# Optimization experiments

Measured on AMD Instinct MI355X. Metric: run time of the kernel, lower is better.

Reference implementation:

```python
import jax, jax.numpy as jnp
import numpy as np

B, IMG, C = 128, 128, 3
NP = 8                      # n_patches per side
PS = IMG // NP              # patch size = 16
IN_D = C * PS * PS          # 768
E, NH, L, A = 768, 12, 12, 256
HS = E // NH                # 64
T = NP * NP + 1             # 65 tokens (cls + patches)
LN_EPS = 1e-5


def _pos_emb(seq_len, d):
    i = np.arange(seq_len, dtype=np.float64)[:, None]
    j = np.arange(d, dtype=np.float64)[None, :]
    even = np.sin(i / 10000 ** (j / d))
    odd = np.cos(i / 10000 ** ((j - 1) / d))
    return jnp.asarray(np.where(j % 2 == 0, even, odd), dtype=jnp.float32)


def setup_inputs() -> dict:
    key = jax.random.key(0)
    ks = jax.random.split(key, 16)
    s_e = 1.0 / np.sqrt(E)
    s_in = 1.0 / np.sqrt(IN_D)
    s_4e = 1.0 / np.sqrt(4 * E)
    return {
        "images": jax.random.normal(ks[0], (B, IMG, IMG, C), jnp.float32),
        "lin_w": jax.random.normal(ks[1], (IN_D, E), jnp.float32) * s_in,
        "cls_tok": jax.random.uniform(ks[2], (1, E), jnp.float32),
        "pos_emb": _pos_emb(T, E),
        "Wq": jax.random.normal(ks[3], (L, E, E), jnp.float32) * s_e,
        "Wk": jax.random.normal(ks[4], (L, E, E), jnp.float32) * s_e,
        "Wv": jax.random.normal(ks[5], (L, E, E), jnp.float32) * s_e,
        "Wo": jax.random.normal(ks[6], (L, E, E), jnp.float32) * s_e,
        "bo": jnp.zeros((L, E), jnp.float32),
        "ln1g": jnp.ones((L, E), jnp.float32),
        "ln1b": jnp.zeros((L, E), jnp.float32),
        "ln2g": jnp.ones((L, E), jnp.float32),
        "ln2b": jnp.zeros((L, E), jnp.float32),
        "W1": jax.random.normal(ks[7], (L, E, 4 * E), jnp.float32) * s_e,
        "b1": jnp.zeros((L, 4 * E), jnp.float32),
        "W2": jax.random.normal(ks[8], (L, 4 * E, E), jnp.float32) * s_4e,
        "b2": jnp.zeros((L, E), jnp.float32),
        "head_w": jax.random.normal(ks[9], (E, A), jnp.float32) * s_e,
        "head_b": jnp.zeros((A,), jnp.float32),
    }


def _layernorm(x, g, b):
    mu = jnp.mean(x, axis=-1, keepdims=True)
    var = jnp.var(x, axis=-1, keepdims=True)
    return (x - mu) * jax.lax.rsqrt(var + LN_EPS) * g + b


def _vit_forward(images, lin_w, cls_tok, pos_emb, Wq, Wk, Wv, Wo, bo,
                 ln1g, ln1b, ln2g, ln2b, W1, b1, W2, b2, head_w, head_b):
    n = images.shape[0]
    # patches: 'b (h p1) (w p2) c -> b (h w) (p1 p2 c)'
    p = images.reshape(n, NP, PS, NP, PS, C)
    patches = p.transpose(0, 1, 3, 2, 4, 5).reshape(n, NP * NP, IN_D)
    x = patches @ lin_w                                   # [B, 64, E]
    x = jnp.concatenate([jnp.broadcast_to(cls_tok, (n, 1, E)), x], axis=1)
    x = x + pos_emb[None]                                 # [B, T, E]

    scale = E ** (-0.5)  # NOTE: original scales by n_embd, not head_size

    def block(x, params):
        wq, wk, wv, wo_, bo_, g1, be1, g2, be2, w1, bb1, w2, bb2 = params
        h = _layernorm(x, g1, be1)
        q = (h @ wq).reshape(n, T, NH, HS)
        k = (h @ wk).reshape(n, T, NH, HS)
        v = (h @ wv).reshape(n, T, NH, HS)
        wei = jnp.einsum('bthd,bshd->bhts', q, k) * scale
        wei = jax.nn.softmax(wei, axis=-1)
        attn = jnp.einsum('bhts,bshd->bthd', wei, v).reshape(n, T, E)
        x = x + attn @ wo_ + bo_
        h2 = _layernorm(x, g2, be2)
        x = x + jax.nn.relu(h2 @ w1 + bb1) @ w2 + bb2
        return x, None

    x, _ = jax.lax.scan(block, x,
                        (Wq, Wk, Wv, Wo, bo, ln1g, ln1b, ln2g, ln2b,
                         W1, b1, W2, b2))
    cls = x[:, 0]                                          # [B, E]
    logits = jax.nn.softmax(cls @ head_w + head_b, axis=-1)  # model ends in Softmax
    return logits


def reference(images, lin_w, cls_tok, pos_emb, Wq, Wk, Wv, Wo, bo,
              ln1g, ln1b, ln2g, ln2b, W1, b1, W2, b2, head_w, head_b):
    return _vit_forward(images, lin_w, cls_tok, pos_emb, Wq, Wk, Wv, Wo, bo,
                        ln1g, ln1b, ln2g, ln2b, W1, b1, W2, b2, head_w, head_b)
```

## Files before the change

### kernel.cpp

```cpp
#include <hip/hip_runtime.h>
#include <cstdint>
#include <cstddef>


typedef __bf16 bf16x8 __attribute__((ext_vector_type(8)));
typedef float  f32x4  __attribute__((ext_vector_type(4)));

#define DEVINL __device__ __forceinline__

DEVINL uint16_t f2bf(float f){
  union U{float f; uint32_t i;} v; v.f=f; uint32_t u=v.i;
  return (uint16_t)((u + 0x7fffu + ((u>>16)&1u)) >> 16);
}

DEVINL void gl_lds16(const void* g, void* l){
  __builtin_amdgcn_global_load_lds((const __attribute__((address_space(1))) void*)g,
                                   (__attribute__((address_space(3))) void*)l, 16, 0, 0);
}

__global__ __launch_bounds__(256) void patchify_k(const float* __restrict__ img,
                                                  uint16_t* __restrict__ out){
  int i = blockIdx.x*256 + threadIdx.x;
  int m  = i / 768, kk = i - m*768;
  int b  = m >> 6,  t  = m & 63;
  int py = t >> 3,  px = t & 7;
  int r  = kk / 48, rem = kk - r*48;
  size_t src = ((size_t)(b*128 + py*16 + r)*128 + px*16)*3 + rem;
  out[i] = f2bf(img[src]);
}

DEVINL void tile_transpose(const float* __restrict__ src, uint16_t* __restrict__ dst,
                           int R, int C, int ti, int tj, int tid){
  __shared__ uint16_t tile[32][33];
  int tx = tid & 31, ty = tid >> 5;
  int r0 = ti*32, c0 = tj*32;
  #pragma unroll
  for (int i=0;i<4;++i)
    tile[ty+i*8][tx] = f2bf(src[(size_t)(r0+ty+i*8)*C + c0 + tx]);
  __syncthreads();
  #pragma unroll
  for (int i=0;i<4;++i)
    dst[(size_t)(c0+ty+i*8)*R + r0 + tx] = tile[tx][ty+i*8];
}

__global__ __launch_bounds__(256) void transpose_cvt_k(const float* __restrict__ src,
                                                       uint16_t* __restrict__ dst, int R, int C){
  tile_transpose(src, dst, R, C, blockIdx.y, blockIdx.x, threadIdx.x);
}

__global__ __launch_bounds__(256) void prep_layer_k(
    const float* __restrict__ Wq, const float* __restrict__ Wk,
    const float* __restrict__ Wv, const float* __restrict__ Wo,
    const float* __restrict__ W1, const float* __restrict__ W2,
    uint16_t* __restrict__ wbuf){
  int idx = blockIdx.x;
  const float* src; uint16_t* dst; int R, C, ti, tj;
  if (idx < 2304){
    int m = idx / 576, t = idx - m*576; ti = t/24; tj = t - ti*24; R=768; C=768;
    src = (m==0)?Wq:(m==1)?Wk:(m==2)?Wv:Wo;
    dst = wbuf + (size_t)m*589824;
  } else if (idx < 4608){
    int t = idx - 2304; ti = t/96; tj = t - ti*96; R=768; C=3072;
    src = W1; dst = wbuf + 2359296;
  } else {
    int t = idx - 4608; ti = t/24; tj = t - ti*24; R=3072; C=768;
    src = W2; dst = wbuf + 4718592;
  }
  tile_transpose(src, dst, R, C, ti, tj, threadIdx.x);
}

__global__ __launch_bounds__(256) void cls_init_k(const float* __restrict__ ct,
                                                  const float* __restrict__ pos,
                                                  float* __restrict__ X){
  int b = blockIdx.x, tid = threadIdx.x;
  for (int e = tid; e < 768; e += 256)
    X[(size_t)b*65*768 + e] = ct[e] + pos[e];
}

__global__ __launch_bounds__(256) void ln_k(const float* __restrict__ Xin,
                                            uint16_t* __restrict__ H,
                                            const float* __restrict__ g,
                                            const float* __restrict__ b){
  int row = blockIdx.x, tid = threadIdx.x;
  const float* xr = Xin + (size_t)row*768;
  float v0 = xr[tid], v1 = xr[tid+256], v2 = xr[tid+512];
  int wid = tid>>6, lane = tid&63;
  __shared__ float part[4];
  __shared__ float bc[2];
  float s = v0+v1+v2;
  #pragma unroll
  for (int o=32;o;o>>=1) s += __shfl_down(s,o);
  if (lane==0) part[wid] = s;
  __syncthreads();
  if (tid==0) bc[0] = (part[0]+part[1]+part[2]+part[3]) * (1.f/768.f);
  __syncthreads();
  float mu = bc[0];
  float d0=v0-mu, d1=v1-mu, d2=v2-mu;
  float q = d0*d0 + d1*d1 + d2*d2;
  #pragma unroll
  for (int o=32;o;o>>=1) q += __shfl_down(q,o);
  __syncthreads();
  if (lane==0) part[wid] = q;
  __syncthreads();
  if (tid==0) bc[1] = rsqrtf((part[0]+part[1]+part[2]+part[3])*(1.f/768.f) + 1e-5f);
  __syncthreads();
  float rs = bc[1];
  uint16_t* hr = H + (size_t)row*768;
  hr[tid]     = f2bf(d0*rs*g[tid]     + b[tid]);
  hr[tid+256] = f2bf(d1*rs*g[tid+256] + b[tid+256]);
  hr[tid+512] = f2bf(d2*rs*g[tid+512] + b[tid+512]);
}

enum { EP_BF16=0, EP_RES=1, EP_RELU=2, EP_EMB=3 };

template<int MODE, int BN>
__global__ __launch_bounds__(256) void gemm_bt_k(
    const uint16_t* __restrict__ A, const uint16_t* __restrict__ Bt,
    int M, int N, int K, int strideB, long long strideO,
    const float* __restrict__ bias, float* __restrict__ X,
    uint16_t* __restrict__ Obf, const float* __restrict__ pos)
{
  constexpr int WN = BN/2;
  constexpr int NF = WN/16;
  constexpr int BLOADS = BN/64;
  __shared__ __align__(16) uint16_t sA[2][128*32];
  __shared__ __align__(16) uint16_t sB[2][BN*32];
  const int tid = threadIdx.x;
  const int wid = tid>>6, lane = tid&63;
  const int nx = gridDim.x;
  const int nwg = nx*gridDim.y;
  {
  }
  int idx = blockIdx.y*nx + blockIdx.x;
  int q8 = nwg>>3, r8 = nwg&7, xcd = idx&7, off = idx>>3;
  int swz = (xcd<r8 ? xcd*(q8+1) : r8*(q8+1) + (xcd-r8)*q8) + off;
  const int bn = (swz % nx)*BN, bm = (swz / nx)*128;
  const int z = blockIdx.z;
  const uint16_t* Bz = Bt + (size_t)z*strideB;
  const int wr = wid>>1, wc = wid&1;
  const int frow = lane&15, g = lane>>4;
  int srA[2], scA[2];
  #pragma unroll
  for (int rr=0; rr<2; ++rr){
    int G = rr*256 + tid;
    srA[rr] = G>>2; scA[rr] = ((G&3) - (G>>3)) & 3;
  }
  int srB[2], scB[2];
  #pragma unroll
  for (int rr=0; rr<BLOADS; ++rr){
    int G = rr*256 + tid;
    srB[rr] = G>>2; scB[rr] = ((G&3) - (G>>3)) & 3;
  }
  const int rsw = (frow>>1)&3;
  f32x4 acc[4][NF] = {};
  const int nt = K>>5;

  #pragma unroll
  for (int rr=0; rr<2; ++rr)
    gl_lds16(A + (size_t)(bm+srA[rr])*K + scA[rr]*8, (char*)sA[0] + (rr*256 + wid*64)*16);
  #pragma unroll
  for (int rr=0; rr<BLOADS; ++rr)
    gl_lds16(Bz + (size_t)(bn+srB[rr])*K + scB[rr]*8, (char*)sB[0] + (rr*256 + wid*64)*16);

  int buf = 0;
  for (int t = 0; t < nt; ++t){
    if (t+1 < nt){
      int k0 = (t+1)<<5;
      #pragma unroll
      for (int rr=0; rr<2; ++rr)
        gl_lds16(A + (size_t)(bm+srA[rr])*K + k0 + scA[rr]*8,
                 (char*)sA[buf^1] + (rr*256 + wid*64)*16);
      #pragma unroll
      for (int rr=0; rr<BLOADS; ++rr)
        gl_lds16(Bz + (size_t)(bn+srB[rr])*K + k0 + scB[rr]*8,
                 (char*)sB[buf^1] + (rr*256 + wid*64)*16);
      if constexpr (BLOADS==1) asm volatile("s_waitcnt vmcnt(3)" ::: "memory");
      else                     asm volatile("s_waitcnt vmcnt(4)" ::: "memory");
    } else {
      asm volatile("s_waitcnt vmcnt(0)" ::: "memory");
    }
    __builtin_amdgcn_s_barrier();
    bf16x8 a[4], b[NF];
    const char* sAc = (const char*)sA[buf];
    const char* sBc = (const char*)sB[buf];
    #pragma unroll
    for (int m=0;m<4;++m)
      a[m] = *(const bf16x8*)(sAc + (wr*64+m*16+frow)*64 + (((g+rsw)&3)<<4));
    #pragma unroll
    for (int n=0;n<NF;++n)
      b[n] = *(const bf16x8*)(sBc + (wc*WN+n*16+frow)*64 + (((g+rsw)&3)<<4));
    #pragma unroll
    for (int m=0;m<4;++m)
      #pragma unroll
      for (int n=0;n<NF;++n)
        acc[m][n] = __builtin_amdgcn_mfma_f32_16x16x32_bf16(a[m], b[n], acc[m][n], 0,0,0);
    __builtin_amdgcn_s_barrier();
    buf ^= 1;
  }

  uint16_t* Oz = Obf + (size_t)z*(size_t)strideO;
  #pragma unroll
  for (int m=0;m<4;++m){
    int gr0 = bm + wr*64 + m*16 + (lane>>4)*4;
    #pragma unroll
    for (int n=0;n<NF;++n){
      int gc = bn + wc*WN + n*16 + (lane&15);
      #pragma unroll
      for (int r=0;r<4;++r){
        int grow = gr0 + r;
        float vsum = acc[m][n][r];
        if constexpr (MODE==EP_BF16){
          Oz[(size_t)grow*N + gc] = f2bf(vsum);
        } else if constexpr (MODE==EP_RES){
          X[(size_t)grow*N + gc] += vsum + bias[gc];
        } else if constexpr (MODE==EP_RELU){
          float u = vsum + bias[gc];
          Oz[(size_t)grow*N + gc] = f2bf(u > 0.f ? u : 0.f);
        } else {
          int t2 = grow & 63, bb = grow >> 6;
          X[((size_t)bb*65 + 1 + t2)*768 + gc] = vsum + pos[(size_t)(t2+1)*768 + gc];
        }
      }
    }
  }
}

__global__ __launch_bounds__(320) void attn_mfma_k(const uint16_t* __restrict__ q,
    const uint16_t* __restrict__ k, const uint16_t* __restrict__ v,
    uint16_t* __restrict__ o)
{
  __shared__ __align__(16) uint16_t P_lds[80][104];
  __shared__ __align__(16) uint16_t Vt[64][104];
  const int bh = blockIdx.x; const int b = bh / 12, hd = bh - b*12;
  const int tid = threadIdx.x;
  const int m = tid>>6;
  const int lane = tid&63;
  const int g = lane>>4, c = lane&15;
  const size_t base = (size_t)b*65*768 + (size_t)hd*64;

  for (int i = tid; i < 80*16; i += 320) P_lds[i>>4][80 + (i&15)] = 0;
  for (int i = tid; i < 64*32; i += 320) Vt[i>>5][64 + (i&31)] = 0;
  __syncthreads();
  for (int j = tid; j < 520; j += 320){
    int key = j >> 3, dc = j & 7;
    union { bf16x8 v8; uint16_t u[8]; } gv;
    gv.v8 = *(const bf16x8*)&v[base + (size_t)key*768 + dc*8];
    #pragma unroll
    for (int e = 0; e < 8; ++e) Vt[dc*8 + e][key] = gv.u[e];
  }

  bf16x8 bk[5][2];
  #pragma unroll
  for (int n=0;n<5;++n)
    #pragma unroll
    for (int kk=0;kk<2;++kk)
      bk[n][kk] = *(const bf16x8*)&k[base + (size_t)(n*16 + c)*768 + kk*32 + g*8];

  bf16x8 aq[2];
  #pragma unroll
  for (int kk=0;kk<2;++kk)
    aq[kk] = *(const bf16x8*)&q[base + (size_t)(m*16 + c)*768 + kk*32 + g*8];
  f32x4 sacc[5] = {};
  #pragma unroll
  for (int kk=0;kk<2;++kk)
    #pragma unroll
    for (int n=0;n<5;++n)
      sacc[n] = __builtin_amdgcn_mfma_f32_16x16x32_bf16(aq[kk], bk[n][kk], sacc[n], 0,0,0);

  const float scale = 0.03608439182435161f;
  #pragma unroll
  for (int r=0;r<4;++r){
    float val[5]; float mx = -3.0e38f;
    #pragma unroll
    for (int n=0;n<5;++n){
      val[n] = (n*16 + c) < 65 ? sacc[n][r]*scale : -3.0e38f;
      mx = fmaxf(mx, val[n]);
    }
    #pragma unroll
    for (int off=1; off<16; off<<=1) mx = fmaxf(mx, __shfl_xor(mx, off));
    float p[5], sum = 0.f;
    #pragma unroll
    for (int n=0;n<5;++n){
      p[n] = (n*16 + c) < 65 ? __expf(val[n]-mx) : 0.f;
      sum += p[n];
    }
    #pragma unroll
    for (int off=1; off<16; off<<=1) sum += __shfl_xor(sum, off);
    float rinv = 1.f / sum;
    int row = m*16 + g*4 + r;
    #pragma unroll
    for (int n=0;n<5;++n) P_lds[row][n*16 + c] = f2bf(p[n]*rinv);
  }
  __syncthreads();

  bf16x8 vb[4][3];
  #pragma unroll
  for (int n=0;n<4;++n)
    #pragma unroll
    for (int kk=0;kk<3;++kk)
      vb[n][kk] = *(const bf16x8*)&Vt[n*16 + c][kk*32 + g*8];
  f32x4 oacc[4] = {};
  #pragma unroll
  for (int kk=0;kk<3;++kk){
    bf16x8 pa = *(const bf16x8*)&P_lds[m*16 + c][kk*32 + g*8];
    #pragma unroll
    for (int n=0;n<4;++n)
      oacc[n] = __builtin_amdgcn_mfma_f32_16x16x32_bf16(pa, vb[n][kk], oacc[n], 0,0,0);
  }
  #pragma unroll
  for (int r=0;r<4;++r){
    int row = m*16 + g*4 + r;
    if (row < 65){
      #pragma unroll
      for (int n=0;n<4;++n)
        o[base + (size_t)row*768 + n*16 + c] = f2bf(oacc[n][r]);
    }
  }
}

__global__ __launch_bounds__(256) void head_k(const float* __restrict__ X,
    const float* __restrict__ W, const float* __restrict__ bias,
    float* __restrict__ out){
  int b = blockIdx.x, a = threadIdx.x;
  const float* xr = X + (size_t)b*65*768;
  float acc = bias[a];
  for (int kk=0; kk<768; ++kk) acc += xr[kk]*W[(size_t)kk*256 + a];
  int wid = a>>6, lane = a&63;
  __shared__ float red[4];
  float mx = acc;
  #pragma unroll
  for (int off=32; off; off>>=1) mx = fmaxf(mx, __shfl_xor(mx, off));
  if (lane==0) red[wid]=mx;
  __syncthreads();
  mx = fmaxf(fmaxf(red[0],red[1]), fmaxf(red[2],red[3]));
  float e = __expf(acc-mx);
  float s = e;
  #pragma unroll
  for (int off=32; off; off>>=1) s += __shfl_xor(s, off);
  __syncthreads();
  if (lane==0) red[wid]=s;
  __syncthreads();
  s = red[0]+red[1]+red[2]+red[3];
  out[(size_t)b*256 + a] = e/s;
}

extern "C" void kernel_launch(void* const* d_in, const int* in_sizes, int n_in,
                              void* d_out, int out_size, void* d_ws, size_t ws_size,
                              hipStream_t stream)
{
  const float* images = (const float*)d_in[0];
  const float* lin_w  = (const float*)d_in[1];
  const float* cls_tok= (const float*)d_in[2];
  const float* pos    = (const float*)d_in[3];
  const float* Wq = (const float*)d_in[4];
  const float* Wk = (const float*)d_in[5];
  const float* Wv = (const float*)d_in[6];
  const float* Wo = (const float*)d_in[7];
  const float* bo = (const float*)d_in[8];
  const float* ln1g=(const float*)d_in[9];
  const float* ln1b=(const float*)d_in[10];
  const float* ln2g=(const float*)d_in[11];
  const float* ln2b=(const float*)d_in[12];
  const float* W1 = (const float*)d_in[13];
  const float* b1 = (const float*)d_in[14];
  const float* W2 = (const float*)d_in[15];
  const float* b2 = (const float*)d_in[16];
  const float* hw = (const float*)d_in[17];
  const float* hb = (const float*)d_in[18];

  char* ws = (char*)d_ws;
  float*    x    = (float*)   (ws + 0);
  uint16_t* h    = (uint16_t*)(ws + 25559040);
  uint16_t* qkv  = (uint16_t*)(ws + 38338560);
  uint16_t* attn = (uint16_t*)(ws + 76677120);
  uint16_t* mid  = (uint16_t*)(ws + 89456640);
  uint16_t* wbuf = (uint16_t*)(ws + 140574720);
  uint16_t* lwt  = (uint16_t*)(ws + 154730496);

  patchify_k<<<24576,256,0,stream>>>(images, mid);
  transpose_cvt_k<<<dim3(24,24),256,0,stream>>>(lin_w, lwt, 768, 768);
  gemm_bt_k<EP_EMB,64><<<dim3(12,64,1),256,0,stream>>>(mid, lwt, 8192,768,768, 0,0,
                                                   nullptr, x, nullptr, pos);
  cls_init_k<<<128,256,0,stream>>>(cls_tok, pos, x);

  for (int l=0;l<12;++l){
    prep_layer_k<<<6912,256,0,stream>>>(Wq+(size_t)l*589824, Wk+(size_t)l*589824,
                                        Wv+(size_t)l*589824, Wo+(size_t)l*589824,
                                        W1+(size_t)l*2359296, W2+(size_t)l*2359296, wbuf);
    ln_k<<<8320,256,0,stream>>>(x, h, ln1g+(size_t)l*768, ln1b+(size_t)l*768);
    gemm_bt_k<EP_BF16,128><<<dim3(6,65,3),256,0,stream>>>(h, wbuf, 8320,768,768,
                                                      589824, 6389760LL,
                                                      nullptr, nullptr, qkv, nullptr);
    attn_mfma_k<<<1536,320,0,stream>>>(qkv, qkv+6389760, qkv+12779520, attn);
    gemm_bt_k<EP_RES,64><<<dim3(12,65,1),256,0,stream>>>(attn, wbuf+1769472, 8320,768,768,
                                                     0,0, bo+(size_t)l*768, x, nullptr, nullptr);
    ln_k<<<8320,256,0,stream>>>(x, h, ln2g+(size_t)l*768, ln2b+(size_t)l*768);
    gemm_bt_k<EP_RELU,128><<<dim3(24,65,1),256,0,stream>>>(h, wbuf+2359296, 8320,3072,768,
                                                       0,0, b1+(size_t)l*3072, nullptr, mid, nullptr);
    gemm_bt_k<EP_RES,64><<<dim3(12,65,1),256,0,stream>>>(mid, wbuf+4718592, 8320,768,3072,
                                                     0,0, b2+(size_t)l*768, x, nullptr, nullptr);
  }
  head_k<<<128,256,0,stream>>>(x, hw, hb, (float*)d_out);
}
```

Baseline: 3.268 ms.

## Split K in two for residual-output GEMMs with atomic accumulation

Adds a split-K template parameter to the GEMM and uses two K-slices for the Wo projection and the W2 down-projection, which write residuals. Each slice atomically adds its partial sum into the fp32 residual buffer, and only slice zero adds the bias. This doubles the workgroup count for these N=768 GEMMs (780 tiles before), aiming at better CU occupancy and latency hiding. The cost is twice the atomic read-modify-write traffic on X and non-deterministic summation order.

```diff
diff --git a/kernel.cpp b/kernel.cpp
--- a/kernel.cpp
+++ b/kernel.cpp
@@ -113,7 +113,7 @@
 
 enum { EP_BF16=0, EP_RES=1, EP_RELU=2, EP_EMB=3 };
 
-template<int MODE, int BN>
+template<int MODE, int BN, int SK>
 __global__ __launch_bounds__(256) void gemm_bt_k(
     const uint16_t* __restrict__ A, const uint16_t* __restrict__ Bt,
     int M, int N, int K, int strideB, long long strideO,
@@ -129,14 +129,14 @@
   const int wid = tid>>6, lane = tid&63;
   const int nx = gridDim.x;
   const int nwg = nx*gridDim.y;
-  {
-  }
   int idx = blockIdx.y*nx + blockIdx.x;
   int q8 = nwg>>3, r8 = nwg&7, xcd = idx&7, off = idx>>3;
   int swz = (xcd<r8 ? xcd*(q8+1) : r8*(q8+1) + (xcd-r8)*q8) + off;
   const int bn = (swz % nx)*BN, bm = (swz / nx)*128;
   const int z = blockIdx.z;
-  const uint16_t* Bz = Bt + (size_t)z*strideB;
+  const uint16_t* Bz = (SK==1) ? Bt + (size_t)z*strideB : Bt;
+  const int kbase = (SK==1) ? 0 : z*(K/SK);
+  const int KS = (SK==1) ? K : K/SK;
   const int wr = wid>>1, wc = wid&1;
   const int frow = lane&15, g = lane>>4;
   int srA[2], scA[2];
@@ -145,7 +145,7 @@
     int G = rr*256 + tid;
     srA[rr] = G>>2; scA[rr] = ((G&3) - (G>>3)) & 3;
   }
-  int srB[2], scB[2];
+  int srB[BLOADS], scB[BLOADS];
   #pragma unroll
   for (int rr=0; rr<BLOADS; ++rr){
     int G = rr*256 + tid;
@@ -153,19 +153,21 @@
   }
   const int rsw = (frow>>1)&3;
   f32x4 acc[4][NF] = {};
-  const int nt = K>>5;
+  const int nt = KS>>5;
 
   #pragma unroll
   for (int rr=0; rr<2; ++rr)
-    gl_lds16(A + (size_t)(bm+srA[rr])*K + scA[rr]*8, (char*)sA[0] + (rr*256 + wid*64)*16);
+    gl_lds16(A + (size_t)(bm+srA[rr])*K + kbase + scA[rr]*8,
+             (char*)sA[0] + (rr*256 + wid*64)*16);
   #pragma unroll
   for (int rr=0; rr<BLOADS; ++rr)
-    gl_lds16(Bz + (size_t)(bn+srB[rr])*K + scB[rr]*8, (char*)sB[0] + (rr*256 + wid*64)*16);
+    gl_lds16(Bz + (size_t)(bn+srB[rr])*K + kbase + scB[rr]*8,
+             (char*)sB[0] + (rr*256 + wid*64)*16);
 
   int buf = 0;
   for (int t = 0; t < nt; ++t){
     if (t+1 < nt){
-      int k0 = (t+1)<<5;
+      int k0 = kbase + ((t+1)<<5);
       #pragma unroll
       for (int rr=0; rr<2; ++rr)
         gl_lds16(A + (size_t)(bm+srA[rr])*K + k0 + scA[rr]*8,
@@ -212,7 +214,11 @@
         if constexpr (MODE==EP_BF16){
           Oz[(size_t)grow*N + gc] = f2bf(vsum);
         } else if constexpr (MODE==EP_RES){
-          X[(size_t)grow*N + gc] += vsum + bias[gc];
+          if constexpr (SK==1){
+            X[(size_t)grow*N + gc] += vsum + bias[gc];
+          } else {
+            atomicAdd(&X[(size_t)grow*N + gc], vsum + (z==0 ? bias[gc] : 0.f));
+          }
         } else if constexpr (MODE==EP_RELU){
           float u = vsum + bias[gc];
           Oz[(size_t)grow*N + gc] = f2bf(u > 0.f ? u : 0.f);
@@ -379,7 +385,7 @@
 
   patchify_k<<<24576,256,0,stream>>>(images, mid);
   transpose_cvt_k<<<dim3(24,24),256,0,stream>>>(lin_w, lwt, 768, 768);
-  gemm_bt_k<EP_EMB,64><<<dim3(12,64,1),256,0,stream>>>(mid, lwt, 8192,768,768, 0,0,
+  gemm_bt_k<EP_EMB,64,1><<<dim3(12,64,1),256,0,stream>>>(mid, lwt, 8192,768,768, 0,0,
                                                    nullptr, x, nullptr, pos);
   cls_init_k<<<128,256,0,stream>>>(cls_tok, pos, x);
 
@@ -388,16 +394,16 @@
                                         Wv+(size_t)l*589824, Wo+(size_t)l*589824,
                                         W1+(size_t)l*2359296, W2+(size_t)l*2359296, wbuf);
     ln_k<<<8320,256,0,stream>>>(x, h, ln1g+(size_t)l*768, ln1b+(size_t)l*768);
-    gemm_bt_k<EP_BF16,128><<<dim3(6,65,3),256,0,stream>>>(h, wbuf, 8320,768,768,
+    gemm_bt_k<EP_BF16,128,1><<<dim3(6,65,3),256,0,stream>>>(h, wbuf, 8320,768,768,
                                                       589824, 6389760LL,
                                                       nullptr, nullptr, qkv, nullptr);
     attn_mfma_k<<<1536,320,0,stream>>>(qkv, qkv+6389760, qkv+12779520, attn);
-    gemm_bt_k<EP_RES,64><<<dim3(12,65,1),256,0,stream>>>(attn, wbuf+1769472, 8320,768,768,
+    gemm_bt_k<EP_RES,64,2><<<dim3(12,65,2),256,0,stream>>>(attn, wbuf+1769472, 8320,768,768,
                                                      0,0, bo+(size_t)l*768, x, nullptr, nullptr);
     ln_k<<<8320,256,0,stream>>>(x, h, ln2g+(size_t)l*768, ln2b+(size_t)l*768);
-    gemm_bt_k<EP_RELU,128><<<dim3(24,65,1),256,0,stream>>>(h, wbuf+2359296, 8320,3072,768,
+    gemm_bt_k<EP_RELU,128,1><<<dim3(24,65,1),256,0,stream>>>(h, wbuf+2359296, 8320,3072,768,
                                                        0,0, b1+(size_t)l*3072, nullptr, mid, nullptr);
-    gemm_bt_k<EP_RES,64><<<dim3(12,65,1),256,0,stream>>>(mid, wbuf+4718592, 8320,768,3072,
+    gemm_bt_k<EP_RES,64,2><<<dim3(12,65,2),256,0,stream>>>(mid, wbuf+4718592, 8320,768,3072,
                                                      0,0, b2+(size_t)l*768, x, nullptr, nullptr);
   }
   head_k<<<128,256,0,stream>>>(x, hw, hb, (float*)d_out);
```

After: 3.878 ms. 1.19x slower.
